# Kernel optimization log

Measured on AMD Instinct MI355X. Metric: run time of the kernel, lower is better.

## Reference

```python
import jax, jax.numpy as jnp
import numpy as np

EPS = 1e-07  # DIoULoss eps


def setup_inputs() -> dict:
    key = jax.random.key(0)
    k1, k2, k3, k4, k5 = jax.random.split(key, 5)
    B, Q = 32, 131072
    # valid xyxy boxes: uniform centers in [0,100), sizes in [1,51)
    def make_boxes(kc, ks):
        c = jax.random.uniform(kc, (B, Q, 2), dtype=jnp.float32) * 100.0
        wh = jax.random.uniform(ks, (B, Q, 2), dtype=jnp.float32) * 50.0 + 1.0
        return jnp.concatenate([c - wh / 2, c + wh / 2], axis=-1)
    inputs = make_boxes(k1, k2)
    targets = make_boxes(k3, k4)
    mask = jax.random.randint(k5, (B, Q), 0, 2).astype(jnp.bool_)
    num_boxes = 2097152
    return {"inputs": inputs, "targets": targets, "mask": mask, "num_boxes": num_boxes}


def _diou_loss(b1, b2):
    # b1, b2: (N, 4) xyxy. Per-pair GIoU == diagonal of the original NxN matrix.
    a1 = (b1[:, 2] - b1[:, 0]) * (b1[:, 3] - b1[:, 1])
    a2 = (b2[:, 2] - b2[:, 0]) * (b2[:, 3] - b2[:, 1])
    lt = jnp.maximum(b1[:, :2], b2[:, :2])
    rb = jnp.minimum(b1[:, 2:], b2[:, 2:])
    wh = jnp.clip(rb - lt, 0.0)
    inter = wh[:, 0] * wh[:, 1]
    union = a1 + a2 - inter
    iou = inter / union
    lt_c = jnp.minimum(b1[:, :2], b2[:, :2])
    rb_c = jnp.maximum(b1[:, 2:], b2[:, 2:])
    wh_c = rb_c - lt_c  # boxes are valid so enclose extent >= 0
    area_c = wh_c[:, 0] * wh_c[:, 1]
    giou = iou - (area_c - union) / area_c
    # DIoU penalty: squared center distance / squared enclosing diagonal
    c1 = (b1[:, :2] + b1[:, 2:]) * 0.5
    c2 = (b2[:, :2] + b2[:, 2:]) * 0.5
    d2 = jnp.sum((c1 - c2) ** 2, axis=1)
    diag2 = wh_c[:, 0] ** 2 + wh_c[:, 1] ** 2
    diou = giou - d2 / (diag2 + EPS)
    return 1.0 - diou


def reference(inputs, targets, mask, num_boxes):
    B, Q, _ = inputs.shape
    loss = _diou_loss(inputs.reshape(-1, 4), targets.reshape(-1, 4)).reshape(B, Q)
    loss = loss * mask.astype(loss.dtype)
    # reduction='mean' with num_boxes provided -> sum / num_boxes
    return loss.sum() / num_boxes
```

## Files before the change

kernel.cpp:

```cpp
#include <hip/hip_runtime.h>

#define DIOU_EPS 1e-7f

constexpr int BLOCK = 256;
constexpr int ITEMS = 4;
constexpr int CHUNK = BLOCK * ITEMS;

__global__ void zero_out_kernel(float* out) {
    out[0] = 0.0f;
}

__device__ __forceinline__ float diou_elem(float4 a, float4 b, int m) {
    float a1 = (a.z - a.x) * (a.w - a.y);
    float a2 = (b.z - b.x) * (b.w - b.y);

    float iw = fmaxf(fminf(a.z, b.z) - fmaxf(a.x, b.x), 0.0f);
    float ih = fmaxf(fminf(a.w, b.w) - fmaxf(a.y, b.y), 0.0f);
    float inter = iw * ih;
    float uni = a1 + a2 - inter;
    float iou = inter / uni;

    float wc = fmaxf(a.z, b.z) - fminf(a.x, b.x);
    float hc = fmaxf(a.w, b.w) - fminf(a.y, b.y);
    float area_c = wc * hc;

    float giou = iou - (area_c - uni) / area_c;

    float dx = (a.x + a.z - b.x - b.z) * 0.5f;
    float dy = (a.y + a.w - b.y - b.w) * 0.5f;
    float d2 = dx * dx + dy * dy;
    float diag2 = wc * wc + hc * hc;

    float diou = giou - d2 / (diag2 + DIOU_EPS);
    float mf = (float)(m != 0);
    return mf * (1.0f - diou);
}

__global__ __launch_bounds__(BLOCK) void diou_loss_kernel(
    const float4* __restrict__ boxes1,
    const float4* __restrict__ boxes2,
    const int* __restrict__ mask,
    const int* __restrict__ num_boxes,
    float* __restrict__ out,
    int n)
{
    const int t = threadIdx.x;
    const int base = blockIdx.x * CHUNK;

    float acc = 0.0f;

    if (base + CHUNK <= n) {
        float4 A[ITEMS], B[ITEMS];
        int    M[ITEMS];
        #pragma unroll
        for (int j = 0; j < ITEMS; ++j) A[j] = boxes1[base + j * BLOCK + t];
        #pragma unroll
        for (int j = 0; j < ITEMS; ++j) B[j] = boxes2[base + j * BLOCK + t];
        #pragma unroll
        for (int j = 0; j < ITEMS; ++j) M[j] = mask[base + j * BLOCK + t];

        #pragma unroll
        for (int j = 0; j < ITEMS; ++j) acc += diou_elem(A[j], B[j], M[j]);
    } else {
        #pragma unroll
        for (int j = 0; j < ITEMS; ++j) {
            int i = base + j * BLOCK + t;
            if (i < n) acc += diou_elem(boxes1[i], boxes2[i], mask[i]);
        }
    }

    #pragma unroll
    for (int off = 32; off > 0; off >>= 1)
        acc += __shfl_down(acc, off, 64);

    __shared__ float wave_sums[BLOCK / 64];
    int wave = t >> 6;
    if ((t & 63) == 0) wave_sums[wave] = acc;
    __syncthreads();

    if (t == 0) {
        float s = wave_sums[0] + wave_sums[1] + wave_sums[2] + wave_sums[3];
        float inv_nb = 1.0f / (float)num_boxes[0];
        atomicAdd(out, s * inv_nb);
    }
}

extern "C" void kernel_launch(void* const* d_in, const int* in_sizes, int n_in,
                              void* d_out, int out_size, void* d_ws, size_t ws_size,
                              hipStream_t stream) {
    const float4* boxes1 = (const float4*)d_in[0];
    const float4* boxes2 = (const float4*)d_in[1];
    const int* mask = (const int*)d_in[2];
    const int* num_boxes = (const int*)d_in[3];

    float* out = (float*)d_out;
    int n = in_sizes[2];

    zero_out_kernel<<<1, 1, 0, stream>>>(out);

    int grid = (n + CHUNK - 1) / CHUNK;
    diou_loss_kernel<<<grid, BLOCK, 0, stream>>>(boxes1, boxes2, mask, num_boxes, out, n);
}
```

Measured before the change: 178.9 us.

## Use persistent grid with prefetching loads, fast reciprocals, and two-pass reduction

Replaces the one-block-per-chunk launch with a fixed 1024-block persistent grid. Each thread processes four contiguous boxes and prefetches the next tile's boxes and packed int4 mask while computing the current one. Divisions are algebraically folded into a single expression using hardware approximate reciprocals. The global atomicAdd and zero-init kernel are replaced by per-block partials in workspace plus a single finalize kernel. This trades some precision from the approximate reciprocal and doubles register use for prefetch buffers, in exchange for fewer blocks, fewer divisions and no atomic contention.

Result: faster. 163.2 us (-8.8%).

```diff
diff --git a/kernel.cpp b/kernel.cpp
--- a/kernel.cpp
+++ b/kernel.cpp
@@ -3,11 +3,12 @@
 #define DIOU_EPS 1e-7f
 
 constexpr int BLOCK = 256;
-constexpr int ITEMS = 4;
-constexpr int CHUNK = BLOCK * ITEMS;
+constexpr int GRID  = 1024;
+constexpr int VPT   = 4;
+constexpr int TILE  = BLOCK * VPT;
 
-__global__ void zero_out_kernel(float* out) {
-    out[0] = 0.0f;
+__device__ __forceinline__ float rcp_fast(float x) {
+    return __builtin_amdgcn_rcpf(x);
 }
 
 __device__ __forceinline__ float diou_elem(float4 a, float4 b, int m) {
@@ -18,71 +19,105 @@
     float ih = fmaxf(fminf(a.w, b.w) - fmaxf(a.y, b.y), 0.0f);
     float inter = iw * ih;
     float uni = a1 + a2 - inter;
-    float iou = inter / uni;
 
     float wc = fmaxf(a.z, b.z) - fminf(a.x, b.x);
     float hc = fmaxf(a.w, b.w) - fminf(a.y, b.y);
     float area_c = wc * hc;
-
-    float giou = iou - (area_c - uni) / area_c;
 
     float dx = (a.x + a.z - b.x - b.z) * 0.5f;
     float dy = (a.y + a.w - b.y - b.w) * 0.5f;
     float d2 = dx * dx + dy * dy;
     float diag2 = wc * wc + hc * hc;
 
-    float diou = giou - d2 / (diag2 + DIOU_EPS);
-    float mf = (float)(m != 0);
-    return mf * (1.0f - diou);
+    float loss = 2.0f - inter * rcp_fast(uni)
+                      - uni   * rcp_fast(area_c)
+                      + d2    * rcp_fast(diag2 + DIOU_EPS);
+
+    return (m != 0) ? loss : 0.0f;
 }
 
-__global__ __launch_bounds__(BLOCK) void diou_loss_kernel(
+struct Tile {
+    float4 A[VPT];
+    float4 B[VPT];
+    int4   M;
+};
+
+__device__ __forceinline__ void load_tile(const float4* __restrict__ boxes1,
+                                          const float4* __restrict__ boxes2,
+                                          const int4* __restrict__ mask4,
+                                          long long e0, Tile& T) {
+    #pragma unroll
+    for (int j = 0; j < VPT; ++j) T.A[j] = boxes1[e0 + j];
+    #pragma unroll
+    for (int j = 0; j < VPT; ++j) T.B[j] = boxes2[e0 + j];
+    T.M = mask4[e0 >> 2];
+}
+
+__global__ __launch_bounds__(BLOCK, 4) void diou_partial_kernel(
     const float4* __restrict__ boxes1,
     const float4* __restrict__ boxes2,
     const int* __restrict__ mask,
-    const int* __restrict__ num_boxes,
-    float* __restrict__ out,
+    float* __restrict__ ws,
     int n)
 {
     const int t = threadIdx.x;
-    const int base = blockIdx.x * CHUNK;
+    const int4* mask4 = (const int4*)mask;
+    const long long nfull = n / TILE;
 
     float acc = 0.0f;
 
-    if (base + CHUNK <= n) {
-        float4 A[ITEMS], B[ITEMS];
-        int    M[ITEMS];
+    Tile cur, nxt;
+    long long tb = blockIdx.x;
+    bool any = tb < nfull;
+    if (any) load_tile(boxes1, boxes2, mask4, tb * TILE + (long long)t * VPT, cur);
+
+    while (any) {
+        long long tn = tb + GRID;
+        bool hn = tn < nfull;
+        if (hn) load_tile(boxes1, boxes2, mask4, tn * TILE + (long long)t * VPT, nxt);
+
+        int mm[VPT] = {cur.M.x, cur.M.y, cur.M.z, cur.M.w};
         #pragma unroll
-        for (int j = 0; j < ITEMS; ++j) A[j] = boxes1[base + j * BLOCK + t];
-        #pragma unroll
-        for (int j = 0; j < ITEMS; ++j) B[j] = boxes2[base + j * BLOCK + t];
-        #pragma unroll
-        for (int j = 0; j < ITEMS; ++j) M[j] = mask[base + j * BLOCK + t];
+        for (int j = 0; j < VPT; ++j) acc += diou_elem(cur.A[j], cur.B[j], mm[j]);
 
-        #pragma unroll
-        for (int j = 0; j < ITEMS; ++j) acc += diou_elem(A[j], B[j], M[j]);
-    } else {
-        #pragma unroll
-        for (int j = 0; j < ITEMS; ++j) {
-            int i = base + j * BLOCK + t;
-            if (i < n) acc += diou_elem(boxes1[i], boxes2[i], mask[i]);
-        }
+        cur = nxt;
+        tb = tn;
+        any = hn;
     }
+
+    for (long long i = nfull * TILE + (long long)blockIdx.x * BLOCK + t; i < n;
+         i += (long long)GRID * BLOCK)
+        acc += diou_elem(boxes1[i], boxes2[i], mask[i]);
 
     #pragma unroll
     for (int off = 32; off > 0; off >>= 1)
         acc += __shfl_down(acc, off, 64);
 
-    __shared__ float wave_sums[BLOCK / 64];
-    int wave = t >> 6;
-    if ((t & 63) == 0) wave_sums[wave] = acc;
+    __shared__ float wsum[BLOCK / 64];
+    if ((t & 63) == 0) wsum[t >> 6] = acc;
     __syncthreads();
+    if (t == 0) ws[blockIdx.x] = wsum[0] + wsum[1] + wsum[2] + wsum[3];
+}
 
-    if (t == 0) {
-        float s = wave_sums[0] + wave_sums[1] + wave_sums[2] + wave_sums[3];
-        float inv_nb = 1.0f / (float)num_boxes[0];
-        atomicAdd(out, s * inv_nb);
-    }
+__global__ __launch_bounds__(BLOCK) void finalize_kernel(
+    const float* __restrict__ ws,
+    const int* __restrict__ num_boxes,
+    float* __restrict__ out)
+{
+    const int t = threadIdx.x;
+    float a = 0.0f;
+    #pragma unroll
+    for (int i = 0; i < GRID / BLOCK; ++i) a += ws[i * BLOCK + t];
+
+    #pragma unroll
+    for (int off = 32; off > 0; off >>= 1)
+        a += __shfl_down(a, off, 64);
+
+    __shared__ float wsum[BLOCK / 64];
+    if ((t & 63) == 0) wsum[t >> 6] = a;
+    __syncthreads();
+    if (t == 0)
+        out[0] = (wsum[0] + wsum[1] + wsum[2] + wsum[3]) / (float)num_boxes[0];
 }
 
 extern "C" void kernel_launch(void* const* d_in, const int* in_sizes, int n_in,
@@ -94,10 +129,9 @@
     const int* num_boxes = (const int*)d_in[3];
 
     float* out = (float*)d_out;
+    float* partials = (float*)d_ws;
     int n = in_sizes[2];
 
-    zero_out_kernel<<<1, 1, 0, stream>>>(out);
-
-    int grid = (n + CHUNK - 1) / CHUNK;
-    diou_loss_kernel<<<grid, BLOCK, 0, stream>>>(boxes1, boxes2, mask, num_boxes, out, n);
+    diou_partial_kernel<<<GRID, BLOCK, 0, stream>>>(boxes1, boxes2, mask, partials, n);
+    finalize_kernel<<<1, BLOCK, 0, stream>>>(partials, num_boxes, out);
 }
```
